# Kernel tuning notes

Measured on AMD Instinct MI355X. Metric: run time of the kernel, lower is better.

Reference implementation:

```python
import jax, jax.numpy as jnp
import numpy as np

N, D, F, O = 32768, 32, 128, 128  # nodes, fixed in-degree, in_feats, out_feats


def _lstm_reduce(m, W_ih, W_hh, b_ih, b_hh):
    """Run an LSTM over each node's neighbor mailbox m: [N, T, F] -> final h: [N, H].
    PyTorch gate order: i, f, g, o. W_ih: [4H, F], W_hh: [4H, H]."""
    n, _, _ = m.shape
    H = W_hh.shape[1]
    b = b_ih + b_hh

    def step(carry, x_t):
        h, c = carry
        gates = x_t @ W_ih.T + h @ W_hh.T + b  # [N, 4H]
        i, f, g, o = jnp.split(gates, 4, axis=-1)
        c = jax.nn.sigmoid(f) * c + jax.nn.sigmoid(i) * jnp.tanh(g)
        h = jax.nn.sigmoid(o) * jnp.tanh(c)
        return (h, c), None

    h0 = jnp.zeros((n, H), m.dtype)
    (h_final, _), _ = jax.lax.scan(step, (h0, h0), jnp.swapaxes(m, 0, 1))
    return h_final


def setup_inputs() -> dict:
    key = jax.random.key(0)
    ks = jax.random.split(key, 9)
    stdv_lin = 1.0 / np.sqrt(F)   # linear init: uniform(-1/sqrt(in_feats))
    stdv_lstm = 1.0 / np.sqrt(F)  # torch LSTM init: uniform(-1/sqrt(hidden))
    u = lambda k, shape, s: jax.random.uniform(k, shape, jnp.float32, -s, s)
    return {
        "feat": jax.random.normal(ks[0], (N, F), jnp.float32),
        "neigh_idx": jax.random.randint(ks[1], (N, D), 0, N, jnp.int32),
        "W_ih": u(ks[2], (4 * F, F), stdv_lstm),
        "W_hh": u(ks[3], (4 * F, F), stdv_lstm),
        "b_ih": u(ks[4], (4 * F,), stdv_lstm),
        "b_hh": u(ks[5], (4 * F,), stdv_lstm),
        "W1": u(ks[6], (O, F), stdv_lin),
        "b1": u(ks[6], (O,), stdv_lin),
        "W2": u(ks[7], (O, F), stdv_lin),
        "b2": u(ks[8], (O,), stdv_lin),
    }


def reference(feat, neigh_idx, W_ih, W_hh, b_ih, b_hh, W1, b1, W2, b2):
    # Mailbox gather: each node's D neighbor feature rows -> [N, D, F]
    m = feat[neigh_idx]
    # LSTM reducer -> final hidden state per node
    h = _lstm_reduce(m, W_ih, W_hh, b_ih, b_hh)  # [N, F]
    degs = jnp.asarray(neigh_idx.shape[1], feat.dtype)  # fixed-degree graph
    ah = h / degs
    # feat = linear1(feat) + linear2(ah)
    return feat @ W1.T + b1 + ah @ W2.T + b2
```

## Files before the change

### kernel.cpp

```cpp
#include <hip/hip_runtime.h>
#include <hip/hip_bf16.h>

#define NN 32768
#define DEG 32
#define FF 128
#define OO 128
#define MB 32

typedef __attribute__((ext_vector_type(8))) short bfrag;
typedef __attribute__((ext_vector_type(4))) float f32x4;

#define K1 1.4426950408889634f

__device__ __forceinline__ unsigned short b16(float x) {
    unsigned u = __float_as_uint(x) + 0x8000u;
    return (unsigned short)(u >> 16);
}
__device__ __forceinline__ bfrag pack8(float4 a, float4 b) {
    bfrag r;
    r[0] = (short)b16(a.x); r[1] = (short)b16(a.y); r[2] = (short)b16(a.z); r[3] = (short)b16(a.w);
    r[4] = (short)b16(b.x); r[5] = (short)b16(b.y); r[6] = (short)b16(b.z); r[7] = (short)b16(b.w);
    return r;
}

__device__ __forceinline__ float fsig(float x, float nb) {
    return __builtin_amdgcn_rcpf(1.0f + __builtin_amdgcn_exp2f(fmaf(-K1, x, nb)));
}
__device__ __forceinline__ float ftanhb(float x, float pb) {
    return fmaf(-2.0f, __builtin_amdgcn_rcpf(1.0f + __builtin_amdgcn_exp2f(fmaf(2.0f * K1, x, pb))), 1.0f);
}
__device__ __forceinline__ float ftanh(float x) {
    return fmaf(-2.0f, __builtin_amdgcn_rcpf(1.0f + __builtin_amdgcn_exp2f(2.0f * K1 * x)), 1.0f);
}

__device__ __forceinline__ void gload16(const void* g, void* l) {
    __builtin_amdgcn_global_load_lds(
        (const __attribute__((address_space(1))) unsigned int*)g,
        (__attribute__((address_space(3))) unsigned int*)l, 16, 0, 0);
}

__global__ void prep_weights(const float* __restrict__ wih, const float* __restrict__ whh,
                             const float* __restrict__ b_ih, const float* __restrict__ b_hh,
                             const float* __restrict__ w1, const float* __restrict__ b1,
                             const float* __restrict__ w2, const float* __restrict__ b2,
                             short* __restrict__ wihb, short* __restrict__ whhb,
                             short* __restrict__ w1b, short* __restrict__ w2b,
                             float* __restrict__ biasg, float* __restrict__ biaso)
{
    int i = blockIdx.x * blockDim.x + threadIdx.x;
    if (i < 512 * 128) { wihb[i] = (short)b16(wih[i]); whhb[i] = (short)b16(whh[i]); }
    if (i < 128 * 128) { w1b[i] = (short)b16(w1[i]); w2b[i] = (short)b16(w2[i] * 0.03125f); }
    if (i < 512) biasg[i] = b_ih[i] + b_hh[i];
    if (i < 128) biaso[i] = b1[i] + b2[i];
}

__global__ void prep_feat(const float* __restrict__ f, short* __restrict__ fb) {
    int i = blockIdx.x * blockDim.x + threadIdx.x;
    const float4* p = reinterpret_cast<const float4*>(f) + (size_t)i * 2;
    float4 a = p[0], b = p[1];
    *reinterpret_cast<bfrag*>(fb + (size_t)i * 8) = pack8(a, b);
}

template<bool BF16F>
__global__ __launch_bounds__(512, 2)
void sage_lstm_kernel(const float* __restrict__ featf, const short* __restrict__ featb,
                      const int* __restrict__ nidx,
                      const short* __restrict__ wihb, const short* __restrict__ whhb,
                      const short* __restrict__ w1b, const short* __restrict__ w2b,
                      const float* __restrict__ biasg, const float* __restrict__ biaso,
                      float* __restrict__ out)
{
    __shared__ short xbuf[2][MB * 128];
    __shared__ short hbuf[2][MB * 128];
    __shared__ int   idx_s[MB * DEG];

    const int tid  = (int)threadIdx.x;
    const int lane = tid & 63;
    const int wave = tid >> 6;
    const int n0   = (int)blockIdx.x * MB;

    const int srow = tid >> 4;
    const int cs   = tid & 15;
    const int chunk = (cs ^ (srow & 7)) * 8;

    idx_s[tid]       = nidx[n0 * DEG + tid];
    idx_s[512 + tid] = nidx[n0 * DEG + 512 + tid];
    {   bfrag z; for (int j = 0; j < 8; ++j) z[j] = 0;
        reinterpret_cast<bfrag*>(hbuf[0])[tid] = z; }

    const int colw = wave * 16 + (lane & 15);
    bfrag wih[4][4], whh[4][4];
#pragma unroll
    for (int g = 0; g < 4; ++g) {
        const short* pih = wihb + (g * 128 + colw) * FF + (lane >> 4) * 8;
        const short* phh = whhb + (g * 128 + colw) * FF + (lane >> 4) * 8;
#pragma unroll
        for (int kt = 0; kt < 4; ++kt) {
            wih[g][kt] = *reinterpret_cast<const bfrag*>(pih + kt * 32);
            whh[g][kt] = *reinterpret_cast<const bfrag*>(phh + kt * 32);
        }
    }
    const float nbi = -K1 * biasg[colw];
    const float nbf = -K1 * biasg[128 + colw];
    const float pbg = 2.0f * K1 * biasg[256 + colw];
    const float nbo = -K1 * biasg[384 + colw];

    __syncthreads();

    char* const x0p = reinterpret_cast<char*>(xbuf[0]);
    char* const x1p = reinterpret_cast<char*>(xbuf[1]);
    char* const h0p = reinterpret_cast<char*>(hbuf[0]);
    char* const h1p = reinterpret_cast<char*>(hbuf[1]);

    if (BF16F) {
        gload16(featb + idx_s[srow * DEG + 0] * FF + chunk, x0p + wave * 1024);
        gload16(featb + idx_s[srow * DEG + 1] * FF + chunk, x1p + wave * 1024);
    } else {
        int sb = (srow * 256 + cs * 16) ^ ((srow & 7) << 4);
        {   const float4* p = reinterpret_cast<const float4*>(featf + idx_s[srow * DEG + 0] * FF + cs * 8);
            *reinterpret_cast<bfrag*>(x0p + sb) = pack8(p[0], p[1]); }
        {   const float4* p = reinterpret_cast<const float4*>(featf + idx_s[srow * DEG + 1] * FF + cs * 8);
            *reinterpret_cast<bfrag*>(x1p + sb) = pack8(p[0], p[1]); }
    }
    __syncthreads();

    const int arow = lane & 15;
    const int asub = (lane >> 4) * 16;
    const int hr0  = (lane >> 4) * 4;
    const int swz  = (arow & 7) << 4;

    auto mm4 = [&](const char* p, int rbase, const bfrag (&W)[4][4],
                   f32x4& vi, f32x4& vf, f32x4& vg, f32x4& vo) {
        bfrag a[4];
#pragma unroll
        for (int kt = 0; kt < 4; ++kt)
            a[kt] = *reinterpret_cast<const bfrag*>(p + ((rbase * 256 + kt * 64 + asub) ^ swz));
#pragma unroll
        for (int kt = 0; kt < 4; ++kt) {
            vi = __builtin_amdgcn_mfma_f32_16x16x32_bf16(a[kt], W[0][kt], vi, 0, 0, 0);
            vf = __builtin_amdgcn_mfma_f32_16x16x32_bf16(a[kt], W[1][kt], vf, 0, 0, 0);
            vg = __builtin_amdgcn_mfma_f32_16x16x32_bf16(a[kt], W[2][kt], vg, 0, 0, 0);
            vo = __builtin_amdgcn_mfma_f32_16x16x32_bf16(a[kt], W[3][kt], vo, 0, 0, 0);
        }
    };

    auto actw = [&](f32x4& gi, f32x4& gf, f32x4& gg, f32x4& go,
                    f32x4& cst, char* hnxt, int rt) {
#pragma unroll
        for (int r = 0; r < 4; ++r) {
            float iv = fsig(gi[r], nbi);
            float fv = fsig(gf[r], nbf);
            float gv = ftanhb(gg[r], pbg);
            float ov = fsig(go[r], nbo);
            float c  = fmaf(fv, cst[r], iv * gv);
            cst[r] = c;
            float h  = ov * ftanh(c);
            int hrow = rt * 16 + hr0 + r;
            int hb   = (hrow * 256 + colw * 2) ^ ((hrow & 7) << 4);
            *reinterpret_cast<unsigned short*>(hnxt + hb) = b16(h);
        }
    };

    auto stage = [&](int t, char* xwr) {
        int node = idx_s[srow * DEG + t];
        if (BF16F) {
            gload16(featb + node * FF + chunk, xwr + wave * 1024);
        } else {
            const float4* p = reinterpret_cast<const float4*>(featf + node * FF + cs * 8);
            int sb = (srow * 256 + cs * 16) ^ ((srow & 7) << 4);
            *reinterpret_cast<bfrag*>(xwr + sb) = pack8(p[0], p[1]);
        }
    };

    const f32x4 zz = {0.f, 0.f, 0.f, 0.f};
    f32x4 cs0 = zz, cs1 = zz;

    f32x4 Ai0, Af0, Ag0, Ao0, Ai1, Af1, Ag1, Ao1;
    f32x4 Bi0, Bf0, Bg0, Bo0, Bi1, Bf1, Bg1, Bo1;

    Ai0 = zz; Af0 = zz; Ag0 = zz; Ao0 = zz;
    mm4(x0p, arow, wih, Ai0, Af0, Ag0, Ao0);
    Ai1 = zz; Af1 = zz; Ag1 = zz; Ao1 = zz;
    mm4(x0p, 16 + arow, wih, Ai1, Af1, Ag1, Ao1);
    __syncthreads();

#define STEP(T, Gi0,Gf0,Gg0,Go0, Gi1,Gf1,Gg1,Go1, Pi0,Pf0,Pg0,Po0, Pi1,Pf1,Pg1,Po1, HCUR,HNXT,XRD,XWR) \
    {                                                                                  \
        if ((T) < DEG - 2) stage((T) + 2, XWR);                                        \
        __builtin_amdgcn_s_setprio(1);                                                 \
        mm4(HCUR, arow, whh, Gi0, Gf0, Gg0, Go0);                                      \
        if ((T) < DEG - 1) {                                                           \
            Pi0 = zz; Pf0 = zz; Pg0 = zz; Po0 = zz;                                    \
            mm4(XRD, arow, wih, Pi0, Pf0, Pg0, Po0);                                   \
        }                                                                              \
        mm4(HCUR, 16 + arow, whh, Gi1, Gf1, Gg1, Go1);                                 \
        if ((T) < DEG - 1) {                                                           \
            Pi1 = zz; Pf1 = zz; Pg1 = zz; Po1 = zz;                                    \
            mm4(XRD, 16 + arow, wih, Pi1, Pf1, Pg1, Po1);                              \
        }                                                                              \
        __builtin_amdgcn_s_setprio(0);                                                 \
        actw(Gi0, Gf0, Gg0, Go0, cs0, HNXT, 0);                                        \
        actw(Gi1, Gf1, Gg1, Go1, cs1, HNXT, 1);                                        \
        __syncthreads();                                                               \
    }

    for (int tt = 0; tt < DEG; tt += 2) {
        STEP(tt,     Ai0,Af0,Ag0,Ao0, Ai1,Af1,Ag1,Ao1,
                     Bi0,Bf0,Bg0,Bo0, Bi1,Bf1,Bg1,Bo1, h0p, h1p, x1p, x0p);
        STEP(tt + 1, Bi0,Bf0,Bg0,Bo0, Bi1,Bf1,Bg1,Bo1,
                     Ai0,Af0,Ag0,Ao0, Ai1,Af1,Ag1,Ao1, h1p, h0p, x0p, x1p);
    }
#undef STEP

    if (BF16F) {
        gload16(featb + (n0 + srow) * FF + chunk, x0p + wave * 1024);
    } else {
        const float4* p = reinterpret_cast<const float4*>(featf + (n0 + srow) * FF + cs * 8);
        int sb = (srow * 256 + cs * 16) ^ ((srow & 7) << 4);
        *reinterpret_cast<bfrag*>(x0p + sb) = pack8(p[0], p[1]);
    }
    __syncthreads();

    bfrag w1f[4], w2f[4];
#pragma unroll
    for (int kt = 0; kt < 4; ++kt) {
        w1f[kt] = *reinterpret_cast<const bfrag*>(w1b + colw * FF + kt * 32 + (lane >> 4) * 8);
        w2f[kt] = *reinterpret_cast<const bfrag*>(w2b + colw * FF + kt * 32 + (lane >> 4) * 8);
    }
    const float bb = biaso[colw];
#pragma unroll
    for (int rt = 0; rt < 2; ++rt) {
        const int rowr = rt * 16 + arow;
        bfrag fa[4], hfa[4];
#pragma unroll
        for (int kt = 0; kt < 4; ++kt) {
            int byte = (rowr * 256 + kt * 64 + asub) ^ swz;
            fa[kt]  = *reinterpret_cast<const bfrag*>(x0p + byte);
            hfa[kt] = *reinterpret_cast<const bfrag*>(h0p + byte);
        }
        f32x4 acc = {0.f, 0.f, 0.f, 0.f};
#pragma unroll
        for (int kt = 0; kt < 4; ++kt) {
            acc = __builtin_amdgcn_mfma_f32_16x16x32_bf16(fa[kt],  w1f[kt], acc, 0, 0, 0);
            acc = __builtin_amdgcn_mfma_f32_16x16x32_bf16(hfa[kt], w2f[kt], acc, 0, 0, 0);
        }
        const int hr0e = (lane >> 4) * 4;
#pragma unroll
        for (int r = 0; r < 4; ++r) {
            int orow = n0 + rt * 16 + hr0e + r;
            out[orow * OO + colw] = acc[r] + bb;
        }
    }
}

extern "C" void kernel_launch(void* const* d_in, const int* in_sizes, int n_in,
                              void* d_out, int out_size, void* d_ws, size_t ws_size,
                              hipStream_t stream)
{
    const float* feat = (const float*)d_in[0];
    const int*   nidx = (const int*)d_in[1];
    const float* W_ih = (const float*)d_in[2];
    const float* W_hh = (const float*)d_in[3];
    const float* b_ih = (const float*)d_in[4];
    const float* b_hh = (const float*)d_in[5];
    const float* W1   = (const float*)d_in[6];
    const float* b1   = (const float*)d_in[7];
    const float* W2   = (const float*)d_in[8];
    const float* b2   = (const float*)d_in[9];
    float* out = (float*)d_out;

    char* ws = (char*)d_ws;
    short* wihb  = (short*)(ws);
    short* whhb  = (short*)(ws + 131072);
    short* w1b   = (short*)(ws + 262144);
    short* w2b   = (short*)(ws + 294912);
    float* biasg = (float*)(ws + 327680);
    float* biaso = (float*)(ws + 329728);
    short* featb = (short*)(ws + 330240);

    const size_t need = 330240 + (size_t)NN * FF * 2;
    const bool bf = ws_size >= need;

    prep_weights<<<256, 256, 0, stream>>>(W_ih, W_hh, b_ih, b_hh, W1, b1, W2, b2,
                                          wihb, whhb, w1b, w2b, biasg, biaso);
    if (bf) {
        prep_feat<<<2048, 256, 0, stream>>>(feat, featb);
        sage_lstm_kernel<true><<<NN / MB, 512, 0, stream>>>(feat, featb, nidx, wihb, whhb,
                                                            w1b, w2b, biasg, biaso, out);
    } else {
        sage_lstm_kernel<false><<<NN / MB, 512, 0, stream>>>(feat, featb, nidx, wihb, whhb,
                                                             w1b, w2b, biasg, biaso, out);
    }
}
```

Baseline: 326.1 us.

## Stagger x/h matmul order across waves and pad hidden-state LDS rows

Even waves compute the input projection for the next step before the recurrent matmul, and odd waves do it after. This staggers MFMA and activation phases across waves so they overlap, replacing the s_setprio approach. Activations are now interleaved right after each recurrent tile instead of after all matmuls. The h buffer uses a padded row stride (136 shorts) instead of an XOR swizzle, and the x swizzle shrinks from 8 to 4 rows. This may cut address math and bank conflicts but changes the LDS conflict patterns and uses slightly more shared memory.

```diff
diff --git a/kernel.cpp b/kernel.cpp
--- a/kernel.cpp
+++ b/kernel.cpp
@@ -6,6 +6,7 @@
 #define FF 128
 #define OO 128
 #define MB 32
+#define HP 136
 
 typedef __attribute__((ext_vector_type(8))) short bfrag;
 typedef __attribute__((ext_vector_type(4))) float f32x4;
@@ -71,7 +72,7 @@
                       float* __restrict__ out)
 {
     __shared__ short xbuf[2][MB * 128];
-    __shared__ short hbuf[2][MB * 128];
+    __shared__ short hbuf[2][MB * HP];
     __shared__ int   idx_s[MB * DEG];
 
     const int tid  = (int)threadIdx.x;
@@ -81,12 +82,20 @@
 
     const int srow = tid >> 4;
     const int cs   = tid & 15;
-    const int chunk = (cs ^ (srow & 7)) * 8;
+    const int chunk = (cs ^ (srow & 3)) * 8;
 
     idx_s[tid]       = nidx[n0 * DEG + tid];
     idx_s[512 + tid] = nidx[n0 * DEG + 512 + tid];
-    {   bfrag z; for (int j = 0; j < 8; ++j) z[j] = 0;
-        reinterpret_cast<bfrag*>(hbuf[0])[tid] = z; }
+
+    char* const x0p = reinterpret_cast<char*>(xbuf[0]);
+    char* const x1p = reinterpret_cast<char*>(xbuf[1]);
+    char* const h0p = reinterpret_cast<char*>(hbuf[0]);
+    char* const h1p = reinterpret_cast<char*>(hbuf[1]);
+
+    {   bfrag z = {0, 0, 0, 0, 0, 0, 0, 0};
+        reinterpret_cast<bfrag*>(h0p)[tid] = z;
+        if (tid < 32) reinterpret_cast<bfrag*>(h0p + 8192)[tid] = z;
+    }
 
     const int colw = wave * 16 + (lane & 15);
     bfrag wih[4][4], whh[4][4];
@@ -107,16 +116,11 @@
 
     __syncthreads();
 
-    char* const x0p = reinterpret_cast<char*>(xbuf[0]);
-    char* const x1p = reinterpret_cast<char*>(xbuf[1]);
-    char* const h0p = reinterpret_cast<char*>(hbuf[0]);
-    char* const h1p = reinterpret_cast<char*>(hbuf[1]);
-
     if (BF16F) {
         gload16(featb + idx_s[srow * DEG + 0] * FF + chunk, x0p + wave * 1024);
         gload16(featb + idx_s[srow * DEG + 1] * FF + chunk, x1p + wave * 1024);
     } else {
-        int sb = (srow * 256 + cs * 16) ^ ((srow & 7) << 4);
+        int sb = (srow * 256 + cs * 16) ^ ((srow & 3) << 4);
         {   const float4* p = reinterpret_cast<const float4*>(featf + idx_s[srow * DEG + 0] * FF + cs * 8);
             *reinterpret_cast<bfrag*>(x0p + sb) = pack8(p[0], p[1]); }
         {   const float4* p = reinterpret_cast<const float4*>(featf + idx_s[srow * DEG + 1] * FF + cs * 8);
@@ -127,14 +131,17 @@
     const int arow = lane & 15;
     const int asub = (lane >> 4) * 16;
     const int hr0  = (lane >> 4) * 4;
-    const int swz  = (arow & 7) << 4;
-
-    auto mm4 = [&](const char* p, int rbase, const bfrag (&W)[4][4],
-                   f32x4& vi, f32x4& vf, f32x4& vg, f32x4& vo) {
+    const int hoff = arow * HP + (lane >> 4) * 8;
+    const int woff = hr0 * HP + colw;
+    const int xoff = (arow * 256 + asub) ^ ((arow & 3) << 4);
+    const bool evenw = (wave & 1) == 0;
+
+    auto mm4h = [&](const short* hb, int rtoff, const bfrag (&W)[4][4],
+                    f32x4& vi, f32x4& vf, f32x4& vg, f32x4& vo) {
         bfrag a[4];
 #pragma unroll
         for (int kt = 0; kt < 4; ++kt)
-            a[kt] = *reinterpret_cast<const bfrag*>(p + ((rbase * 256 + kt * 64 + asub) ^ swz));
+            a[kt] = *reinterpret_cast<const bfrag*>(hb + rtoff + kt * 32);
 #pragma unroll
         for (int kt = 0; kt < 4; ++kt) {
             vi = __builtin_amdgcn_mfma_f32_16x16x32_bf16(a[kt], W[0][kt], vi, 0, 0, 0);
@@ -143,9 +150,23 @@
             vo = __builtin_amdgcn_mfma_f32_16x16x32_bf16(a[kt], W[3][kt], vo, 0, 0, 0);
         }
     };
+    auto mm4x = [&](const char* xb, int rtoff, const bfrag (&W)[4][4],
+                    f32x4& vi, f32x4& vf, f32x4& vg, f32x4& vo) {
+        bfrag a[4];
+#pragma unroll
+        for (int kt = 0; kt < 4; ++kt)
+            a[kt] = *reinterpret_cast<const bfrag*>(xb + rtoff + kt * 64);
+#pragma unroll
+        for (int kt = 0; kt < 4; ++kt) {
+            vi = __builtin_amdgcn_mfma_f32_16x16x32_bf16(a[kt], W[0][kt], vi, 0, 0, 0);
+            vf = __builtin_amdgcn_mfma_f32_16x16x32_bf16(a[kt], W[1][kt], vf, 0, 0, 0);
+            vg = __builtin_amdgcn_mfma_f32_16x16x32_bf16(a[kt], W[2][kt], vg, 0, 0, 0);
+            vo = __builtin_amdgcn_mfma_f32_16x16x32_bf16(a[kt], W[3][kt], vo, 0, 0, 0);
+        }
+    };
 
     auto actw = [&](f32x4& gi, f32x4& gf, f32x4& gg, f32x4& go,
-                    f32x4& cst, char* hnxt, int rt) {
+                    f32x4& cst, short* hw, int rt) {
 #pragma unroll
         for (int r = 0; r < 4; ++r) {
             float iv = fsig(gi[r], nbi);
@@ -155,9 +176,7 @@
             float c  = fmaf(fv, cst[r], iv * gv);
             cst[r] = c;
             float h  = ov * ftanh(c);
-            int hrow = rt * 16 + hr0 + r;
-            int hb   = (hrow * 256 + colw * 2) ^ ((hrow & 7) << 4);
-            *reinterpret_cast<unsigned short*>(hnxt + hb) = b16(h);
+            hw[(rt * 16 + r) * HP] = (short)b16(h);
         }
     };
 
@@ -167,7 +186,7 @@
             gload16(featb + node * FF + chunk, xwr + wave * 1024);
         } else {
             const float4* p = reinterpret_cast<const float4*>(featf + node * FF + cs * 8);
-            int sb = (srow * 256 + cs * 16) ^ ((srow & 7) << 4);
+            int sb = (srow * 256 + cs * 16) ^ ((srow & 3) << 4);
             *reinterpret_cast<bfrag*>(xwr + sb) = pack8(p[0], p[1]);
         }
     };
@@ -179,28 +198,42 @@
     f32x4 Bi0, Bf0, Bg0, Bo0, Bi1, Bf1, Bg1, Bo1;
 
     Ai0 = zz; Af0 = zz; Ag0 = zz; Ao0 = zz;
-    mm4(x0p, arow, wih, Ai0, Af0, Ag0, Ao0);
+    mm4x(x0p + xoff, 0, wih, Ai0, Af0, Ag0, Ao0);
     Ai1 = zz; Af1 = zz; Ag1 = zz; Ao1 = zz;
-    mm4(x0p, 16 + arow, wih, Ai1, Af1, Ag1, Ao1);
+    mm4x(x0p + xoff, 4096, wih, Ai1, Af1, Ag1, Ao1);
     __syncthreads();
 
 #define STEP(T, Gi0,Gf0,Gg0,Go0, Gi1,Gf1,Gg1,Go1, Pi0,Pf0,Pg0,Po0, Pi1,Pf1,Pg1,Po1, HCUR,HNXT,XRD,XWR) \
     {                                                                                  \
         if ((T) < DEG - 2) stage((T) + 2, XWR);                                        \
-        __builtin_amdgcn_s_setprio(1);                                                 \
-        mm4(HCUR, arow, whh, Gi0, Gf0, Gg0, Go0);                                      \
-        if ((T) < DEG - 1) {                                                           \
-            Pi0 = zz; Pf0 = zz; Pg0 = zz; Po0 = zz;                                    \
-            mm4(XRD, arow, wih, Pi0, Pf0, Pg0, Po0);                                   \
+        const short* hb = reinterpret_cast<const short*>(HCUR) + hoff;                 \
+        short*       hw = reinterpret_cast<short*>(HNXT) + woff;                       \
+        const char*  xb = (XRD) + xoff;                                                \
+        if (evenw) {                                                                   \
+            if ((T) < DEG - 1) {                                                       \
+                Pi0 = zz; Pf0 = zz; Pg0 = zz; Po0 = zz;                                \
+                mm4x(xb, 0, wih, Pi0, Pf0, Pg0, Po0);                                  \
+                Pi1 = zz; Pf1 = zz; Pg1 = zz; Po1 = zz;                                \
+                mm4x(xb, 4096, wih, Pi1, Pf1, Pg1, Po1);                               \
+            }                                                                          \
+            __builtin_amdgcn_sched_barrier(0);                                         \
+            mm4h(hb, 0, whh, Gi0, Gf0, Gg0, Go0);                                      \
+            actw(Gi0, Gf0, Gg0, Go0, cs0, hw, 0);                                      \
+            mm4h(hb, 16 * HP, whh, Gi1, Gf1, Gg1, Go1);                                \
+            actw(Gi1, Gf1, Gg1, Go1, cs1, hw, 1);                                      \
+        } else {                                                                       \
+            mm4h(hb, 0, whh, Gi0, Gf0, Gg0, Go0);                                      \
+            actw(Gi0, Gf0, Gg0, Go0, cs0, hw, 0);                                      \
+            mm4h(hb, 16 * HP, whh, Gi1, Gf1, Gg1, Go1);                                \
+            actw(Gi1, Gf1, Gg1, Go1, cs1, hw, 1);                                      \
+            __builtin_amdgcn_sched_barrier(0);                                         \
+            if ((T) < DEG - 1) {                                                       \
+                Pi0 = zz; Pf0 = zz; Pg0 = zz; Po0 = zz;                                \
+                mm4x(xb, 0, wih, Pi0, Pf0, Pg0, Po0);                                  \
+                Pi1 = zz; Pf1 = zz; Pg1 = zz; Po1 = zz;                                \
+                mm4x(xb, 4096, wih, Pi1, Pf1, Pg1, Po1);                               \
+            }                                                                          \
         }                                                                              \
-        mm4(HCUR, 16 + arow, whh, Gi1, Gf1, Gg1, Go1);                                 \
-        if ((T) < DEG - 1) {                                                           \
-            Pi1 = zz; Pf1 = zz; Pg1 = zz; Po1 = zz;                                    \
-            mm4(XRD, 16 + arow, wih, Pi1, Pf1, Pg1, Po1);                              \
-        }                                                                              \
-        __builtin_amdgcn_s_setprio(0);                                                 \
-        actw(Gi0, Gf0, Gg0, Go0, cs0, HNXT, 0);                                        \
-        actw(Gi1, Gf1, Gg1, Go1, cs1, HNXT, 1);                                        \
         __syncthreads();                                                               \
     }
 
@@ -216,7 +249,7 @@
         gload16(featb + (n0 + srow) * FF + chunk, x0p + wave * 1024);
     } else {
         const float4* p = reinterpret_cast<const float4*>(featf + (n0 + srow) * FF + cs * 8);
-        int sb = (srow * 256 + cs * 16) ^ ((srow & 7) << 4);
+        int sb = (srow * 256 + cs * 16) ^ ((srow & 3) << 4);
         *reinterpret_cast<bfrag*>(x0p + sb) = pack8(p[0], p[1]);
     }
     __syncthreads();
@@ -230,13 +263,12 @@
     const float bb = biaso[colw];
 #pragma unroll
     for (int rt = 0; rt < 2; ++rt) {
-        const int rowr = rt * 16 + arow;
         bfrag fa[4], hfa[4];
 #pragma unroll
         for (int kt = 0; kt < 4; ++kt) {
-            int byte = (rowr * 256 + kt * 64 + asub) ^ swz;
-            fa[kt]  = *reinterpret_cast<const bfrag*>(x0p + byte);
-            hfa[kt] = *reinterpret_cast<const bfrag*>(h0p + byte);
+            fa[kt]  = *reinterpret_cast<const bfrag*>(x0p + xoff + rt * 4096 + kt * 64);
+            hfa[kt] = *reinterpret_cast<const bfrag*>(reinterpret_cast<const short*>(h0p)
+                                                      + hoff + rt * 16 * HP + kt * 32);
         }
         f32x4 acc = {0.f, 0.f, 0.f, 0.f};
 #pragma unroll
@@ -244,10 +276,9 @@
             acc = __builtin_amdgcn_mfma_f32_16x16x32_bf16(fa[kt],  w1f[kt], acc, 0, 0, 0);
             acc = __builtin_amdgcn_mfma_f32_16x16x32_bf16(hfa[kt], w2f[kt], acc, 0, 0, 0);
         }
-        const int hr0e = (lane >> 4) * 4;
 #pragma unroll
         for (int r = 0; r < 4; ++r) {
-            int orow = n0 + rt * 16 + hr0e + r;
+            int orow = n0 + rt * 16 + hr0 + r;
             out[orow * OO + colw] = acc[r] + bb;
         }
     }
```

Measured after the change: 334.6 us. +2.6%, slower.

## Stagger wave groups so half compute input projections while others run recurrence

Applied to the files above, without the earlier changes.

Splits the 8 waves into two groups with opposite phase order inside each LSTM step. The high group computes the next step's input-projection MFMAs first and then the recurrent MFMAs plus activations, while the low group does the reverse. Each group also interleaves the recurrent MFMAs with activations per row tile, with sched barriers and priority hints in between. The aim is to overlap matrix-core work of one group with transcendental/VALU work of the other, at the cost of code duplication and loops that are no longer unrolled.

```diff
diff --git a/kernel.cpp b/kernel.cpp
--- a/kernel.cpp
+++ b/kernel.cpp
@@ -85,7 +85,7 @@
 
     idx_s[tid]       = nidx[n0 * DEG + tid];
     idx_s[512 + tid] = nidx[n0 * DEG + 512 + tid];
-    {   bfrag z; for (int j = 0; j < 8; ++j) z[j] = 0;
+    {   bfrag z = {0, 0, 0, 0, 0, 0, 0, 0};
         reinterpret_cast<bfrag*>(hbuf[0])[tid] = z; }
 
     const int colw = wave * 16 + (lane & 15);
@@ -128,6 +128,7 @@
     const int asub = (lane >> 4) * 16;
     const int hr0  = (lane >> 4) * 4;
     const int swz  = (arow & 7) << 4;
+    const bool hi4 = ((wave >> 2) & 1) != 0;
 
     auto mm4 = [&](const char* p, int rbase, const bfrag (&W)[4][4],
                    f32x4& vi, f32x4& vf, f32x4& vg, f32x4& vo) {
@@ -184,33 +185,63 @@
     mm4(x0p, 16 + arow, wih, Ai1, Af1, Ag1, Ao1);
     __syncthreads();
 
-#define STEP(T, Gi0,Gf0,Gg0,Go0, Gi1,Gf1,Gg1,Go1, Pi0,Pf0,Pg0,Po0, Pi1,Pf1,Pg1,Po1, HCUR,HNXT,XRD,XWR) \
-    {                                                                                  \
-        if ((T) < DEG - 2) stage((T) + 2, XWR);                                        \
-        __builtin_amdgcn_s_setprio(1);                                                 \
-        mm4(HCUR, arow, whh, Gi0, Gf0, Gg0, Go0);                                      \
+#define PCL(T, Pi0,Pf0,Pg0,Po0, Pi1,Pf1,Pg1,Po1, XRD)                                  \
         if ((T) < DEG - 1) {                                                           \
             Pi0 = zz; Pf0 = zz; Pg0 = zz; Po0 = zz;                                    \
             mm4(XRD, arow, wih, Pi0, Pf0, Pg0, Po0);                                   \
-        }                                                                              \
-        mm4(HCUR, 16 + arow, whh, Gi1, Gf1, Gg1, Go1);                                 \
-        if ((T) < DEG - 1) {                                                           \
             Pi1 = zz; Pf1 = zz; Pg1 = zz; Po1 = zz;                                    \
             mm4(XRD, 16 + arow, wih, Pi1, Pf1, Pg1, Po1);                              \
-        }                                                                              \
+        }
+
+#define GACT(Gi0,Gf0,Gg0,Go0, Gi1,Gf1,Gg1,Go1, HCUR,HNXT)                              \
+        __builtin_amdgcn_s_setprio(1);                                                 \
+        mm4(HCUR, arow, whh, Gi0, Gf0, Gg0, Go0);                                      \
         __builtin_amdgcn_s_setprio(0);                                                 \
         actw(Gi0, Gf0, Gg0, Go0, cs0, HNXT, 0);                                        \
-        actw(Gi1, Gf1, Gg1, Go1, cs1, HNXT, 1);                                        \
+        __builtin_amdgcn_s_setprio(1);                                                 \
+        mm4(HCUR, 16 + arow, whh, Gi1, Gf1, Gg1, Go1);                                 \
+        __builtin_amdgcn_s_setprio(0);                                                 \
+        actw(Gi1, Gf1, Gg1, Go1, cs1, HNXT, 1);
+
+#define STEP_HI(T, Gi0,Gf0,Gg0,Go0, Gi1,Gf1,Gg1,Go1, Pi0,Pf0,Pg0,Po0, Pi1,Pf1,Pg1,Po1, HCUR,HNXT,XRD,XWR) \
+    {                                                                                  \
+        if ((T) < DEG - 2) stage((T) + 2, XWR);                                        \
+        PCL(T, Pi0,Pf0,Pg0,Po0, Pi1,Pf1,Pg1,Po1, XRD)                                  \
+        __builtin_amdgcn_sched_barrier(0);                                             \
+        GACT(Gi0,Gf0,Gg0,Go0, Gi1,Gf1,Gg1,Go1, HCUR,HNXT)                              \
         __syncthreads();                                                               \
     }
 
-    for (int tt = 0; tt < DEG; tt += 2) {
-        STEP(tt,     Ai0,Af0,Ag0,Ao0, Ai1,Af1,Ag1,Ao1,
-                     Bi0,Bf0,Bg0,Bo0, Bi1,Bf1,Bg1,Bo1, h0p, h1p, x1p, x0p);
-        STEP(tt + 1, Bi0,Bf0,Bg0,Bo0, Bi1,Bf1,Bg1,Bo1,
-                     Ai0,Af0,Ag0,Ao0, Ai1,Af1,Ag1,Ao1, h1p, h0p, x0p, x1p);
-    }
-#undef STEP
+#define STEP_LO(T, Gi0,Gf0,Gg0,Go0, Gi1,Gf1,Gg1,Go1, Pi0,Pf0,Pg0,Po0, Pi1,Pf1,Pg1,Po1, HCUR,HNXT,XRD,XWR) \
+    {                                                                                  \
+        if ((T) < DEG - 2) stage((T) + 2, XWR);                                        \
+        GACT(Gi0,Gf0,Gg0,Go0, Gi1,Gf1,Gg1,Go1, HCUR,HNXT)                              \
+        __builtin_amdgcn_sched_barrier(0);                                             \
+        PCL(T, Pi0,Pf0,Pg0,Po0, Pi1,Pf1,Pg1,Po1, XRD)                                  \
+        __syncthreads();                                                               \
+    }
+
+    if (hi4) {
+#pragma unroll 1
+        for (int tt = 0; tt < DEG; tt += 2) {
+            STEP_HI(tt,     Ai0,Af0,Ag0,Ao0, Ai1,Af1,Ag1,Ao1,
+                            Bi0,Bf0,Bg0,Bo0, Bi1,Bf1,Bg1,Bo1, h0p, h1p, x1p, x0p);
+            STEP_HI(tt + 1, Bi0,Bf0,Bg0,Bo0, Bi1,Bf1,Bg1,Bo1,
+                            Ai0,Af0,Ag0,Ao0, Ai1,Af1,Ag1,Ao1, h1p, h0p, x0p, x1p);
+        }
+    } else {
+#pragma unroll 1
+        for (int tt = 0; tt < DEG; tt += 2) {
+            STEP_LO(tt,     Ai0,Af0,Ag0,Ao0, Ai1,Af1,Ag1,Ao1,
+                            Bi0,Bf0,Bg0,Bo0, Bi1,Bf1,Bg1,Bo1, h0p, h1p, x1p, x0p);
+            STEP_LO(tt + 1, Bi0,Bf0,Bg0,Bo0, Bi1,Bf1,Bg1,Bo1,
+                            Ai0,Af0,Ag0,Ao0, Ai1,Af1,Ag1,Ao1, h1p, h0p, x0p, x1p);
+        }
+    }
+#undef STEP_HI
+#undef STEP_LO
+#undef GACT
+#undef PCL
 
     if (BF16F) {
         gload16(featb + (n0 + srow) * FF + chunk, x0p + wave * 1024);
@@ -244,10 +275,9 @@
             acc = __builtin_amdgcn_mfma_f32_16x16x32_bf16(fa[kt],  w1f[kt], acc, 0, 0, 0);
             acc = __builtin_amdgcn_mfma_f32_16x16x32_bf16(hfa[kt], w2f[kt], acc, 0, 0, 0);
         }
-        const int hr0e = (lane >> 4) * 4;
 #pragma unroll
         for (int r = 0; r < 4; ++r) {
-            int orow = n0 + rt * 16 + hr0e + r;
+            int orow = n0 + rt * 16 + hr0 + r;
             out[orow * OO + colw] = acc[r] + bb;
         }
     }
```

New measurement: 306.6 us. 1.06x faster.

## Fold LSTM bias into MFMA accumulator init and interleave activation with next tile's MFMAs

Applied to the files above, without the earlier changes.

Merges the LDS buffers into one array with constant offsets and precomputed swizzled base pointers, so address math becomes immediate offsets. The gate bias now seeds the MFMA accumulator instead of being added inside the activations. The step is reordered so the row-tile-0 activation runs between the two row-tiles' MFMA groups, letting transcendental work overlap matrix work. The setprio hints are dropped and the time loop is no longer unrolled, which lowers code size but may cost scheduling freedom.

```diff
diff --git a/kernel.cpp b/kernel.cpp
--- a/kernel.cpp
+++ b/kernel.cpp
@@ -7,6 +7,11 @@
 #define OO 128
 #define MB 32
 
+#define X0B 0
+#define X1B 8192
+#define H0B 16384
+#define H1B 24576
+
 typedef __attribute__((ext_vector_type(8))) short bfrag;
 typedef __attribute__((ext_vector_type(4))) float f32x4;
 
@@ -23,11 +28,8 @@
     return r;
 }
 
-__device__ __forceinline__ float fsig(float x, float nb) {
-    return __builtin_amdgcn_rcpf(1.0f + __builtin_amdgcn_exp2f(fmaf(-K1, x, nb)));
-}
-__device__ __forceinline__ float ftanhb(float x, float pb) {
-    return fmaf(-2.0f, __builtin_amdgcn_rcpf(1.0f + __builtin_amdgcn_exp2f(fmaf(2.0f * K1, x, pb))), 1.0f);
+__device__ __forceinline__ float fsig(float x) {
+    return __builtin_amdgcn_rcpf(1.0f + __builtin_amdgcn_exp2f(-K1 * x));
 }
 __device__ __forceinline__ float ftanh(float x) {
     return fmaf(-2.0f, __builtin_amdgcn_rcpf(1.0f + __builtin_amdgcn_exp2f(2.0f * K1 * x)), 1.0f);
@@ -70,9 +72,8 @@
                       const float* __restrict__ biasg, const float* __restrict__ biaso,
                       float* __restrict__ out)
 {
-    __shared__ short xbuf[2][MB * 128];
-    __shared__ short hbuf[2][MB * 128];
-    __shared__ int   idx_s[MB * DEG];
+    __shared__ char lds[32768];
+    __shared__ int  idx_s[MB * DEG];
 
     const int tid  = (int)threadIdx.x;
     const int lane = tid & 63;
@@ -85,8 +86,8 @@
 
     idx_s[tid]       = nidx[n0 * DEG + tid];
     idx_s[512 + tid] = nidx[n0 * DEG + 512 + tid];
-    {   bfrag z; for (int j = 0; j < 8; ++j) z[j] = 0;
-        reinterpret_cast<bfrag*>(hbuf[0])[tid] = z; }
+    {   bfrag z = {0, 0, 0, 0, 0, 0, 0, 0};
+        *reinterpret_cast<bfrag*>(lds + H0B + tid * 16) = z; }
 
     const int colw = wave * 16 + (lane & 15);
     bfrag wih[4][4], whh[4][4];
@@ -100,27 +101,26 @@
             whh[g][kt] = *reinterpret_cast<const bfrag*>(phh + kt * 32);
         }
     }
-    const float nbi = -K1 * biasg[colw];
-    const float nbf = -K1 * biasg[128 + colw];
-    const float pbg = 2.0f * K1 * biasg[256 + colw];
-    const float nbo = -K1 * biasg[384 + colw];
+    const float bi_ = biasg[colw];
+    const float bf_ = biasg[128 + colw];
+    const float bg_ = biasg[256 + colw];
+    const float bo_ = biasg[384 + colw];
+    const f32x4 BVI = {bi_, bi_, bi_, bi_};
+    const f32x4 BVF = {bf_, bf_, bf_, bf_};
+    const f32x4 BVG = {bg_, bg_, bg_, bg_};
+    const f32x4 BVO = {bo_, bo_, bo_, bo_};
 
     __syncthreads();
 
-    char* const x0p = reinterpret_cast<char*>(xbuf[0]);
-    char* const x1p = reinterpret_cast<char*>(xbuf[1]);
-    char* const h0p = reinterpret_cast<char*>(hbuf[0]);
-    char* const h1p = reinterpret_cast<char*>(hbuf[1]);
-
     if (BF16F) {
-        gload16(featb + idx_s[srow * DEG + 0] * FF + chunk, x0p + wave * 1024);
-        gload16(featb + idx_s[srow * DEG + 1] * FF + chunk, x1p + wave * 1024);
+        gload16(featb + idx_s[srow * DEG + 0] * FF + chunk, lds + X0B + wave * 1024);
+        gload16(featb + idx_s[srow * DEG + 1] * FF + chunk, lds + X1B + wave * 1024);
     } else {
         int sb = (srow * 256 + cs * 16) ^ ((srow & 7) << 4);
         {   const float4* p = reinterpret_cast<const float4*>(featf + idx_s[srow * DEG + 0] * FF + cs * 8);
-            *reinterpret_cast<bfrag*>(x0p + sb) = pack8(p[0], p[1]); }
+            *reinterpret_cast<bfrag*>(lds + X0B + sb) = pack8(p[0], p[1]); }
         {   const float4* p = reinterpret_cast<const float4*>(featf + idx_s[srow * DEG + 1] * FF + cs * 8);
-            *reinterpret_cast<bfrag*>(x1p + sb) = pack8(p[0], p[1]); }
+            *reinterpret_cast<bfrag*>(lds + X1B + sb) = pack8(p[0], p[1]); }
     }
     __syncthreads();
 
@@ -129,46 +129,77 @@
     const int hr0  = (lane >> 4) * 4;
     const int swz  = (arow & 7) << 4;
 
-    auto mm4 = [&](const char* p, int rbase, const bfrag (&W)[4][4],
-                   f32x4& vi, f32x4& vf, f32x4& vg, f32x4& vo) {
-        bfrag a[4];
-#pragma unroll
-        for (int kt = 0; kt < 4; ++kt)
-            a[kt] = *reinterpret_cast<const bfrag*>(p + ((rbase * 256 + kt * 64 + asub) ^ swz));
+    const char* const pA = lds + ((arow * 256 + asub) ^ swz);
+    const char* const pB = lds + ((arow * 256 + 64 + asub) ^ swz);
+    char* hw[4];
+#pragma unroll
+    for (int r = 0; r < 4; ++r) {
+        int hrow = hr0 + r;
+        hw[r] = lds + ((hrow * 256 + colw * 2) ^ ((hrow & 7) << 4));
+    }
+
+    auto mm4_new = [&](int off, const bfrag (&W)[4][4],
+                       f32x4& vi, f32x4& vf, f32x4& vg, f32x4& vo) {
+        bfrag a0 = *reinterpret_cast<const bfrag*>(pA + off);
+        bfrag a1 = *reinterpret_cast<const bfrag*>(pB + off);
+        bfrag a2 = *reinterpret_cast<const bfrag*>(pA + off + 128);
+        bfrag a3 = *reinterpret_cast<const bfrag*>(pB + off + 128);
+        vi = __builtin_amdgcn_mfma_f32_16x16x32_bf16(a0, W[0][0], BVI, 0, 0, 0);
+        vf = __builtin_amdgcn_mfma_f32_16x16x32_bf16(a0, W[1][0], BVF, 0, 0, 0);
+        vg = __builtin_amdgcn_mfma_f32_16x16x32_bf16(a0, W[2][0], BVG, 0, 0, 0);
+        vo = __builtin_amdgcn_mfma_f32_16x16x32_bf16(a0, W[3][0], BVO, 0, 0, 0);
+        vi = __builtin_amdgcn_mfma_f32_16x16x32_bf16(a1, W[0][1], vi, 0, 0, 0);
+        vf = __builtin_amdgcn_mfma_f32_16x16x32_bf16(a1, W[1][1], vf, 0, 0, 0);
+        vg = __builtin_amdgcn_mfma_f32_16x16x32_bf16(a1, W[2][1], vg, 0, 0, 0);
+        vo = __builtin_amdgcn_mfma_f32_16x16x32_bf16(a1, W[3][1], vo, 0, 0, 0);
+        vi = __builtin_amdgcn_mfma_f32_16x16x32_bf16(a2, W[0][2], vi, 0, 0, 0);
+        vf = __builtin_amdgcn_mfma_f32_16x16x32_bf16(a2, W[1][2], vf, 0, 0, 0);
+        vg = __builtin_amdgcn_mfma_f32_16x16x32_bf16(a2, W[2][2], vg, 0, 0, 0);
+        vo = __builtin_amdgcn_mfma_f32_16x16x32_bf16(a2, W[3][2], vo, 0, 0, 0);
+        vi = __builtin_amdgcn_mfma_f32_16x16x32_bf16(a3, W[0][3], vi, 0, 0, 0);
+        vf = __builtin_amdgcn_mfma_f32_16x16x32_bf16(a3, W[1][3], vf, 0, 0, 0);
+        vg = __builtin_amdgcn_mfma_f32_16x16x32_bf16(a3, W[2][3], vg, 0, 0, 0);
+        vo = __builtin_amdgcn_mfma_f32_16x16x32_bf16(a3, W[3][3], vo, 0, 0, 0);
+    };
+    auto mm4_acc = [&](int off, const bfrag (&W)[4][4],
+                       f32x4& vi, f32x4& vf, f32x4& vg, f32x4& vo) {
+        bfrag a0 = *reinterpret_cast<const bfrag*>(pA + off);
+        bfrag a1 = *reinterpret_cast<const bfrag*>(pB + off);
+        bfrag a2 = *reinterpret_cast<const bfrag*>(pA + off + 128);
+        bfrag a3 = *reinterpret_cast<const bfrag*>(pB + off + 128);
 #pragma unroll
         for (int kt = 0; kt < 4; ++kt) {
-            vi = __builtin_amdgcn_mfma_f32_16x16x32_bf16(a[kt], W[0][kt], vi, 0, 0, 0);
-            vf = __builtin_amdgcn_mfma_f32_16x16x32_bf16(a[kt], W[1][kt], vf, 0, 0, 0);
-            vg = __builtin_amdgcn_mfma_f32_16x16x32_bf16(a[kt], W[2][kt], vg, 0, 0, 0);
-            vo = __builtin_amdgcn_mfma_f32_16x16x32_bf16(a[kt], W[3][kt], vo, 0, 0, 0);
+            bfrag a = kt == 0 ? a0 : kt == 1 ? a1 : kt == 2 ? a2 : a3;
+            vi = __builtin_amdgcn_mfma_f32_16x16x32_bf16(a, W[0][kt], vi, 0, 0, 0);
+            vf = __builtin_amdgcn_mfma_f32_16x16x32_bf16(a, W[1][kt], vf, 0, 0, 0);
+            vg = __builtin_amdgcn_mfma_f32_16x16x32_bf16(a, W[2][kt], vg, 0, 0, 0);
+            vo = __builtin_amdgcn_mfma_f32_16x16x32_bf16(a, W[3][kt], vo, 0, 0, 0);
         }
     };
 
     auto actw = [&](f32x4& gi, f32x4& gf, f32x4& gg, f32x4& go,
-                    f32x4& cst, char* hnxt, int rt) {
+                    f32x4& cst, int woff) {
 #pragma unroll
         for (int r = 0; r < 4; ++r) {
-            float iv = fsig(gi[r], nbi);
-            float fv = fsig(gf[r], nbf);
-            float gv = ftanhb(gg[r], pbg);
-            float ov = fsig(go[r], nbo);
+            float iv = fsig(gi[r]);
+            float fv = fsig(gf[r]);
+            float gv = ftanh(gg[r]);
+            float ov = fsig(go[r]);
             float c  = fmaf(fv, cst[r], iv * gv);
             cst[r] = c;
             float h  = ov * ftanh(c);
-            int hrow = rt * 16 + hr0 + r;
-            int hb   = (hrow * 256 + colw * 2) ^ ((hrow & 7) << 4);
-            *reinterpret_cast<unsigned short*>(hnxt + hb) = b16(h);
+            *reinterpret_cast<unsigned short*>(hw[r] + woff) = b16(h);
         }
     };
 
-    auto stage = [&](int t, char* xwr) {
+    auto stage = [&](int t, int xwrb) {
         int node = idx_s[srow * DEG + t];
         if (BF16F) {
-            gload16(featb + node * FF + chunk, xwr + wave * 1024);
+            gload16(featb + node * FF + chunk, lds + xwrb + wave * 1024);
         } else {
             const float4* p = reinterpret_cast<const float4*>(featf + node * FF + cs * 8);
             int sb = (srow * 256 + cs * 16) ^ ((srow & 7) << 4);
-            *reinterpret_cast<bfrag*>(xwr + sb) = pack8(p[0], p[1]);
+            *reinterpret_cast<bfrag*>(lds + xwrb + sb) = pack8(p[0], p[1]);
         }
     };
 
@@ -178,46 +209,37 @@
     f32x4 Ai0, Af0, Ag0, Ao0, Ai1, Af1, Ag1, Ao1;
     f32x4 Bi0, Bf0, Bg0, Bo0, Bi1, Bf1, Bg1, Bo1;
 
-    Ai0 = zz; Af0 = zz; Ag0 = zz; Ao0 = zz;
-    mm4(x0p, arow, wih, Ai0, Af0, Ag0, Ao0);
-    Ai1 = zz; Af1 = zz; Ag1 = zz; Ao1 = zz;
-    mm4(x0p, 16 + arow, wih, Ai1, Af1, Ag1, Ao1);
+    mm4_new(X0B,        wih, Ai0, Af0, Ag0, Ao0);
+    mm4_new(X0B + 4096, wih, Ai1, Af1, Ag1, Ao1);
     __syncthreads();
 
-#define STEP(T, Gi0,Gf0,Gg0,Go0, Gi1,Gf1,Gg1,Go1, Pi0,Pf0,Pg0,Po0, Pi1,Pf1,Pg1,Po1, HCUR,HNXT,XRD,XWR) \
+#define STEP(T, Gi0,Gf0,Gg0,Go0, Gi1,Gf1,Gg1,Go1, Pi0,Pf0,Pg0,Po0, Pi1,Pf1,Pg1,Po1, HCURB,HNXTB,XRDB,XWRB) \
     {                                                                                  \
-        if ((T) < DEG - 2) stage((T) + 2, XWR);                                        \
-        __builtin_amdgcn_s_setprio(1);                                                 \
-        mm4(HCUR, arow, whh, Gi0, Gf0, Gg0, Go0);                                      \
-        if ((T) < DEG - 1) {                                                           \
-            Pi0 = zz; Pf0 = zz; Pg0 = zz; Po0 = zz;                                    \
-            mm4(XRD, arow, wih, Pi0, Pf0, Pg0, Po0);                                   \
-        }                                                                              \
-        mm4(HCUR, 16 + arow, whh, Gi1, Gf1, Gg1, Go1);                                 \
-        if ((T) < DEG - 1) {                                                           \
-            Pi1 = zz; Pf1 = zz; Pg1 = zz; Po1 = zz;                                    \
-            mm4(XRD, 16 + arow, wih, Pi1, Pf1, Pg1, Po1);                              \
-        }                                                                              \
-        __builtin_amdgcn_s_setprio(0);                                                 \
-        actw(Gi0, Gf0, Gg0, Go0, cs0, HNXT, 0);                                        \
-        actw(Gi1, Gf1, Gg1, Go1, cs1, HNXT, 1);                                        \
+        if ((T) < DEG - 2) stage((T) + 2, XWRB);                                       \
+        mm4_acc(HCURB, whh, Gi0, Gf0, Gg0, Go0);                                       \
+        if ((T) < DEG - 1) mm4_new(XRDB, wih, Pi0, Pf0, Pg0, Po0);                     \
+        actw(Gi0, Gf0, Gg0, Go0, cs0, HNXTB);                                          \
+        mm4_acc(HCURB + 4096, whh, Gi1, Gf1, Gg1, Go1);                                \
+        if ((T) < DEG - 1) mm4_new(XRDB + 4096, wih, Pi1, Pf1, Pg1, Po1);              \
+        actw(Gi1, Gf1, Gg1, Go1, cs1, HNXTB + 4096);                                   \
         __syncthreads();                                                               \
     }
 
+#pragma unroll 1
     for (int tt = 0; tt < DEG; tt += 2) {
         STEP(tt,     Ai0,Af0,Ag0,Ao0, Ai1,Af1,Ag1,Ao1,
-                     Bi0,Bf0,Bg0,Bo0, Bi1,Bf1,Bg1,Bo1, h0p, h1p, x1p, x0p);
+                     Bi0,Bf0,Bg0,Bo0, Bi1,Bf1,Bg1,Bo1, H0B, H1B, X1B, X0B);
         STEP(tt + 1, Bi0,Bf0,Bg0,Bo0, Bi1,Bf1,Bg1,Bo1,
-                     Ai0,Af0,Ag0,Ao0, Ai1,Af1,Ag1,Ao1, h1p, h0p, x0p, x1p);
+                     Ai0,Af0,Ag0,Ao0, Ai1,Af1,Ag1,Ao1, H1B, H0B, X0B, X1B);
     }
 #undef STEP
 
     if (BF16F) {
-        gload16(featb + (n0 + srow) * FF + chunk, x0p + wave * 1024);
+        gload16(featb + (n0 + srow) * FF + chunk, lds + X0B + wave * 1024);
     } else {
         const float4* p = reinterpret_cast<const float4*>(featf + (n0 + srow) * FF + cs * 8);
         int sb = (srow * 256 + cs * 16) ^ ((srow & 7) << 4);
-        *reinterpret_cast<bfrag*>(x0p + sb) = pack8(p[0], p[1]);
+        *reinterpret_cast<bfrag*>(lds + X0B + sb) = pack8(p[0], p[1]);
     }
     __syncthreads();
 
@@ -230,24 +252,25 @@
     const float bb = biaso[colw];
 #pragma unroll
     for (int rt = 0; rt < 2; ++rt) {
-        const int rowr = rt * 16 + arow;
+        const int off = rt * 4096;
         bfrag fa[4], hfa[4];
-#pragma unroll
-        for (int kt = 0; kt < 4; ++kt) {
-            int byte = (rowr * 256 + kt * 64 + asub) ^ swz;
-            fa[kt]  = *reinterpret_cast<const bfrag*>(x0p + byte);
-            hfa[kt] = *reinterpret_cast<const bfrag*>(h0p + byte);
-        }
+        fa[0]  = *reinterpret_cast<const bfrag*>(pA + X0B + off);
+        fa[1]  = *reinterpret_cast<const bfrag*>(pB + X0B + off);
+        fa[2]  = *reinterpret_cast<const bfrag*>(pA + X0B + off + 128);
+        fa[3]  = *reinterpret_cast<const bfrag*>(pB + X0B + off + 128);
+        hfa[0] = *reinterpret_cast<const bfrag*>(pA + H0B + off);
+        hfa[1] = *reinterpret_cast<const bfrag*>(pB + H0B + off);
+        hfa[2] = *reinterpret_cast<const bfrag*>(pA + H0B + off + 128);
+        hfa[3] = *reinterpret_cast<const bfrag*>(pB + H0B + off + 128);
         f32x4 acc = {0.f, 0.f, 0.f, 0.f};
 #pragma unroll
         for (int kt = 0; kt < 4; ++kt) {
             acc = __builtin_amdgcn_mfma_f32_16x16x32_bf16(fa[kt],  w1f[kt], acc, 0, 0, 0);
             acc = __builtin_amdgcn_mfma_f32_16x16x32_bf16(hfa[kt], w2f[kt], acc, 0, 0, 0);
         }
-        const int hr0e = (lane >> 4) * 4;
 #pragma unroll
         for (int r = 0; r < 4; ++r) {
-            int orow = n0 + rt * 16 + hr0e + r;
+            int orow = n0 + rt * 16 + hr0 + r;
             out[orow * OO + colw] = acc[r] + bb;
         }
     }
```

Result: no change. 320.8 us (-1.6%).
